# Kernel optimization log

Hardware: AMD Instinct MI355X
Metric: run time of the kernel (lower is better)

Reference implementation:

```python
import jax, jax.numpy as jnp
import numpy as np

B = 4096
L = 15          # self.length
NINP = 256      # emb_size
NHID = 512      # hidden_size
VOCAB = 30005
TOPK = 10
K = 4 * TOPK + 2   # 42 actions
N_SPLIT = 2 * TOPK
N_STEP = 5      # num_edits
PAD = 30003


def _lstm_dir(x, Wih, Whh, b, reverse):
    # x: [T,B,D]; Wih: [4H,D]; Whh: [4H,H]; b: [4H] (b_ih+b_hh). PyTorch gate order i,f,g,o.
    Bsz, H = x.shape[1], Whh.shape[1]
    def step(carry, xt):
        h, c = carry
        z = xt @ Wih.T + h @ Whh.T + b
        i, f, g, o = jnp.split(z, 4, axis=-1)
        c = jax.nn.sigmoid(f) * c + jax.nn.sigmoid(i) * jnp.tanh(g)
        h = jax.nn.sigmoid(o) * jnp.tanh(c)
        return (h, c), h
    h0 = jnp.zeros((Bsz, H), x.dtype)
    _, ys = jax.lax.scan(step, (h0, h0), x, reverse=reverse)
    return ys  # [T,B,H], position-aligned for both directions


def bilstm(x, Wih0, Whh0, b0, Wih1, Whh1, b1):
    # x: [B,T,D] -> [B,T,2H]; 2-layer bidirectional, zero initial state (matches c0/h0 zeros).
    xt = jnp.swapaxes(x, 0, 1)
    for Wih, Whh, b in ((Wih0, Whh0, b0), (Wih1, Whh1, b1)):
        fw = _lstm_dir(xt, Wih[0], Whh[0], b[0], False)
        bw = _lstm_dir(xt, Wih[1], Whh[1], b[1], True)
        xt = jnp.concatenate([fw, bw], axis=-1)
    return jnp.swapaxes(xt, 0, 1)


def policy_step(st_1, length_t, pos, emb0, key_pos, rep_words, valid_id,
                emb_table, enc_table, Wih0, Whh0, b0, Wih1, Whh1, b1,
                del_vec, hold_vec, mlp_W, mlp_b, mlp1_W, mlp1_b):
    Bsz = st_1.shape[0]
    pos_row = jnp.zeros((L,), jnp.float32).at[pos].set(1.0)         # static pos
    pos_tensor = jnp.broadcast_to(pos_row[None, :, None], (Bsz, L, 1))
    embt = emb_table[st_1] * (1.0 - pos_tensor)
    x = jnp.concatenate([embt, emb0, pos_tensor], axis=2)            # [B,L,2*ninp+1]
    out = bilstm(x, Wih0, Whh0, b0, Wih1, Whh1, b1)                  # [B,L,2*nhid]
    pooled = out[:, pos, :]
    representation = jnp.concatenate(
        [pooled, key_pos[:, pos:pos + 1], jnp.broadcast_to(pos_row[None, :], (Bsz, L))], axis=1)
    # external encoder output is detached in the original
    word_emb = jax.lax.stop_gradient(enc_table[rep_words])           # [B,4*topk,ninp]
    emb2 = jnp.concatenate([word_emb,
                            jnp.broadcast_to(del_vec, (Bsz, 1, NINP)),
                            jnp.broadcast_to(hold_vec, (Bsz, 1, NINP))], axis=1)  # [B,K,ninp]
    onehot = jnp.broadcast_to(jnp.eye(K, dtype=jnp.float32)[None], (Bsz, K, K))
    emb2 = jnp.concatenate([emb2, onehot], axis=2)                   # [B,K,ninp+K]
    rep100 = representation @ mlp_W.T + mlp_b                        # [B,100]
    emb100 = emb2 @ mlp1_W.T + mlp1_b                                # [B,K,100]
    score = jnp.einsum('bkd,bd->bk', emb100, rep100)
    policy = jax.nn.softmax(score, axis=1)
    action = jnp.argmax(policy, axis=1, keepdims=True).astype(jnp.int32)  # eval mode
    pi = jnp.take_along_axis(policy, action, axis=1)                 # [B,1]

    rep_b = (action < N_SPLIT).astype(jnp.int32)
    replaceflag = rep_b * valid_id
    ins_b = ((action >= N_SPLIT) & (action < 2 * N_SPLIT)).astype(jnp.int32)
    insertflag = ins_b * valid_id * (length_t + ins_b <= 15).astype(jnp.int32)
    del_b = (action == 2 * N_SPLIT).astype(jnp.int32)
    deleteflag = del_b * valid_id * (length_t - del_b > 2).astype(jnp.int32)
    holdflag = 1 - replaceflag - insertflag - deleteflag

    action_words = jnp.take_along_axis(rep_words, jnp.clip(action, 0, N_SPLIT - 1), axis=1)  # [B,1]
    rep_seq = jnp.concatenate([action_words, st_1[:, pos + 1:]], axis=1)
    ins_seq = jnp.concatenate([action_words, st_1[:, pos:-1]], axis=1)
    padding = jnp.full((Bsz, 1), PAD, dtype=st_1.dtype)
    del_seq = jnp.concatenate([st_1[:, pos + 1:], padding], axis=1)
    hol_seq = st_1[:, pos:]
    new_tail = (rep_seq * replaceflag + ins_seq * insertflag
                + del_seq * deleteflag + hol_seq * holdflag)
    st = st_1.at[:, pos:].set(new_tail)
    length_tt = insertflag + length_t - deleteflag
    return st, pi, action.astype(jnp.float32), length_tt


def setup_inputs() -> dict:
    key = jax.random.key(0)
    ks = jax.random.split(key, 20)
    s = 0.05
    in0 = 2 * NINP + 1
    in1 = 2 * NHID
    inp = {
        'input_ids': jax.random.randint(ks[0], (B, L), 0, 30000, dtype=jnp.int32),
        'key_pos': jax.random.uniform(ks[1], (B, L), dtype=jnp.float32),
        'sequence_length': jax.random.randint(ks[2], (B, 1), 3, 16, dtype=jnp.int32),
        'rep_words_all': jax.random.randint(ks[3], (B, N_STEP, 4 * TOPK), 0, 30000, dtype=jnp.int32),
        'valid_id_all': jax.random.randint(ks[4], (B, N_STEP, 1), 0, 2, dtype=jnp.int32),
        'emb_table': jax.random.normal(ks[5], (VOCAB, NINP), jnp.float32) * s,
        'enc_table': jax.random.normal(ks[6], (VOCAB, NINP), jnp.float32) * s,
        'Wih0': jax.random.normal(ks[7], (2, 4 * NHID, in0), jnp.float32) * s,
        'Whh0': jax.random.normal(ks[8], (2, 4 * NHID, NHID), jnp.float32) * s,
        'b0': jax.random.normal(ks[9], (2, 4 * NHID), jnp.float32) * s,
        'Wih1': jax.random.normal(ks[10], (2, 4 * NHID, in1), jnp.float32) * s,
        'Whh1': jax.random.normal(ks[11], (2, 4 * NHID, NHID), jnp.float32) * s,
        'b1': jax.random.normal(ks[12], (2, 4 * NHID), jnp.float32) * s,
        'del_vec': jax.random.uniform(ks[13], (1, 1, NINP), dtype=jnp.float32),
        'hold_vec': jax.random.uniform(ks[14], (1, 1, NINP), dtype=jnp.float32),
        'mlp_W': jax.random.normal(ks[15], (100, 2 * NHID + 1 + L), jnp.float32) * s,
        'mlp_b': jnp.zeros((100,), jnp.float32),
        'mlp1_W': jax.random.normal(ks[16], (100, NINP + K), jnp.float32) * s,
        'mlp1_b': jnp.zeros((100,), jnp.float32),
    }
    return inp


def reference(input_ids, key_pos, sequence_length, rep_words_all, valid_id_all,
              emb_table, enc_table, Wih0, Whh0, b0, Wih1, Whh1, b1,
              del_vec, hold_vec, mlp_W, mlp_b, mlp1_W, mlp1_b):
    st = input_ids
    emb0 = emb_table[input_ids]            # embedding of s0, computed once
    length_t = sequence_length
    pis, acts = [], []
    for i in range(N_STEP):
        pos = i % (L - 3) + 2              # static per unrolled step
        st, pi, a, length_t = policy_step(
            st, length_t, pos, emb0, key_pos,
            rep_words_all[:, i, :], valid_id_all[:, i, :],
            emb_table, enc_table, Wih0, Whh0, b0, Wih1, Whh1, b1,
            del_vec, hold_vec, mlp_W, mlp_b, mlp1_W, mlp1_b)
        pis.append(pi)
        acts.append(a)
    pis = jnp.concatenate(pis, axis=1)     # [B,N_STEP]
    actions = jnp.concatenate(acts, axis=1)
    return pis, actions, st, length_t
```

## Files before the change

### kernel.cpp

```cpp
#include <hip/hip_runtime.h>

#define B_ 4096
#define L_ 15
#define NSTEP_ 5
#define VOC_ 30005
#define PAD_ 30003

typedef _Float16 f16;
typedef f16  f16x8 __attribute__((ext_vector_type(8)));
typedef float f32x16 __attribute__((ext_vector_type(16)));

__device__ __forceinline__ float sigf(float x){ return 1.0f/(1.0f+expf(-x)); }

#define MFMA_(d,a,b) d = __builtin_amdgcn_mfma_f32_32x32x16_f16(a,b,d,0,0,0)

__device__ __forceinline__ void gll16(const f16* g, f16* l){
  __builtin_amdgcn_global_load_lds(
      (const __attribute__((address_space(1))) void*)g,
      (__attribute__((address_space(3))) void*)l, 16, 0, 0);
}

struct RecParams {
  const f16 *A1h_0,*A1l_0,*A1h_1,*A1l_1;
  const f16 *A2h_0,*A2l_0,*A2h_1,*A2l_1;
  const f16 *Wfh_0,*Wfl_0,*Wfh_1,*Wfl_1;
  const float *bias_0,*bias_1;
  const f16 *embH,*embL,*flagpg;
  const int *st,*ids;
  float *c_0,*c_1,*h2_0,*h2_1;
  f16 *hh_0,*hl_0,*hh_1,*hl_1;
  int lda1, lda2, ldh, ldh2, k1p, k2p, first, gather, t_0, t_1, pos, b0c, act0, act1;
};

__device__ __forceinline__ int swz(int row, int s){
  int u = ((row&7)<<1) | s;
  return ((row>>3)<<8) + ((u ^ (u>>1))<<4);
}

__global__ __launch_bounds__(256,2) void rec_gemm(RecParams p){
  const int bxe = blockIdx.x;
  const int ct4 = bxe & 15;
  const int dir = bxe >> 4;
  if (!(dir ? p.act1 : p.act0)) return;
  const f16* A1h = dir ? p.A1h_1 : p.A1h_0;
  const f16* A1l = dir ? p.A1l_1 : p.A1l_0;
  const f16* A2h = dir ? p.A2h_1 : p.A2h_0;
  const f16* A2l = dir ? p.A2l_1 : p.A2l_0;
  const f16* Wfh = dir ? p.Wfh_1 : p.Wfh_0;
  const f16* Wfl = dir ? p.Wfl_1 : p.Wfl_0;
  const float* bias = dir ? p.bias_1 : p.bias_0;
  float* cbuf = dir ? p.c_1 : p.c_0;
  float* h2   = dir ? p.h2_1 : p.h2_0;
  f16* hhb = dir ? p.hh_1 : p.hh_0;
  f16* hlb = dir ? p.hl_1 : p.hl_0;
  const int tcur = dir ? p.t_1 : p.t_0;

  const int tid  = threadIdx.x;
  const int lane = tid & 63;
  const int w    = tid >> 6;
  const int mbase = blockIdx.y*128;

  __shared__ union {
    float z[128*128];
    f16   stg[3][4][2048];
  } sm;

  f32x16 accM[2][2], accX[2][2];
#pragma unroll
  for (int i=0;i<2;i++)
#pragma unroll
    for (int j=0;j<2;j++)
#pragma unroll
      for (int r=0;r<16;r++){ accM[i][j][r]=0.f; accX[i][j][r]=0.f; }

  const int arow = (w&1)*64 + (lane&31);
  const int fs = lane>>5;
  const int aoff0 = swz(arow,    fs), aoff1 = swz(arow+32, fs);

  const int ct0 = ct4*4 + (w>>1)*2;
  const f16* WfhL = Wfh + (size_t)lane*8;
  const f16* WflL = Wfl + (size_t)lane*8;

  int ug = tid & 15; ug ^= ug>>1; ug ^= ug>>2;
  const int rowS = ((tid>>4)<<3) + (ug>>1);
  const int sS   = ug & 1;
  const int ktot = p.k1p + p.k2p;

  int tokT=0, tokI=0, zflag=0;
  if (p.gather){
    int gb = p.b0c + mbase + rowS;
    tokT = p.st [gb*L_ + tcur];
    tokI = p.ids[gb*L_ + tcur];
    zflag = (tcur == p.pos) ? 1 : 0;
  }
  const f16* zeros = p.flagpg + 8;
  const f16* ones0 = p.flagpg;

  auto stage = [&](int ph, int buf){
    f16* d0 = &sm.stg[buf][0][w<<9];
    f16* d1 = &sm.stg[buf][1][w<<9];
    f16* d2 = &sm.stg[buf][2][w<<9];
    f16* d3 = &sm.stg[buf][3][w<<9];
    if (ph < p.k1p){
      if (p.gather){
        if (ph < 8){
          if (zflag){ gll16(zeros,d0); gll16(zeros,d1); gll16(zeros,d2); gll16(zeros,d3); }
          else {
            size_t base = (size_t)tokT*256 + ph*32 + sS*8;
            gll16(p.embH+base, d0); gll16(p.embL+base, d1);
            gll16(p.embH+base+16, d2); gll16(p.embL+base+16, d3);
          }
        } else if (ph < 16){
          size_t base = (size_t)tokI*256 + (ph-8)*32 + sS*8;
          gll16(p.embH+base, d0); gll16(p.embL+base, d1);
          gll16(p.embH+base+16, d2); gll16(p.embL+base+16, d3);
        } else {
          const f16* s0 = (sS==0 && zflag) ? ones0 : zeros;
          gll16(s0,d0); gll16(zeros,d1); gll16(zeros,d2); gll16(zeros,d3);
        }
      } else {
        long base = (long)(mbase+rowS)*p.lda1 + ph*32 + sS*8;
        gll16(A1h+base, d0); gll16(A1l+base, d1);
        gll16(A1h+base+16, d2); gll16(A1l+base+16, d3);
      }
    } else {
      long base = (long)(mbase+rowS)*p.lda2 + (ph - p.k1p)*32 + sS*8;
      gll16(A2h+base, d0); gll16(A2l+base, d1);
      gll16(A2h+base+16, d2); gll16(A2l+base+16, d3);
    }
  };
  auto loadB = [&](int kt16, f16x8* r){
    size_t base = ((size_t)kt16*64 + ct0)*512;
    r[0] = *(const f16x8*)(WfhL + base);
    r[1] = *(const f16x8*)(WfhL + base + 512);
    r[2] = *(const f16x8*)(WflL + base);
    r[3] = *(const f16x8*)(WflL + base + 512);
  };

  f16x8 rb0[4], rb1[4];
  stage(0,0); stage(1,1);
  loadB(0, rb0);
  asm volatile("s_waitcnt vmcnt(8)" ::: "memory");
  __builtin_amdgcn_s_barrier();
  __builtin_amdgcn_sched_barrier(0);

  int bR = 0;
  for (int ph=0; ph<ktot; ++ph){
    const char* s0h = (const char*)sm.stg[bR][0];
    const char* s0l = (const char*)sm.stg[bR][1];
    const char* s1h = (const char*)sm.stg[bR][2];
    const char* s1l = (const char*)sm.stg[bR][3];
    f16x8 a00h = *(const f16x8*)(s0h + aoff0);
    f16x8 a01h = *(const f16x8*)(s0h + aoff1);
    f16x8 a00l = *(const f16x8*)(s0l + aoff0);
    f16x8 a01l = *(const f16x8*)(s0l + aoff1);
    f16x8 a10h = *(const f16x8*)(s1h + aoff0);
    f16x8 a11h = *(const f16x8*)(s1h + aoff1);
    f16x8 a10l = *(const f16x8*)(s1l + aoff0);
    f16x8 a11l = *(const f16x8*)(s1l + aoff1);
    loadB(2*ph+1, rb1);
    if (ph+2 < ktot) stage(ph+2, (bR+2>=3)?(bR-1):(bR+2));
    __builtin_amdgcn_s_setprio(1);
    MFMA_(accM[0][0], a00h, rb0[0]); MFMA_(accX[0][0], a00h, rb0[2]); MFMA_(accX[0][0], a00l, rb0[0]);
    MFMA_(accM[1][0], a01h, rb0[0]); MFMA_(accX[1][0], a01h, rb0[2]); MFMA_(accX[1][0], a01l, rb0[0]);
    MFMA_(accM[0][1], a00h, rb0[1]); MFMA_(accX[0][1], a00h, rb0[3]); MFMA_(accX[0][1], a00l, rb0[1]);
    MFMA_(accM[1][1], a01h, rb0[1]); MFMA_(accX[1][1], a01h, rb0[3]); MFMA_(accX[1][1], a01l, rb0[1]);
    MFMA_(accM[0][0], a10h, rb1[0]); MFMA_(accX[0][0], a10h, rb1[2]); MFMA_(accX[0][0], a10l, rb1[0]);
    MFMA_(accM[1][0], a11h, rb1[0]); MFMA_(accX[1][0], a11h, rb1[2]); MFMA_(accX[1][0], a11l, rb1[0]);
    MFMA_(accM[0][1], a10h, rb1[1]); MFMA_(accX[0][1], a10h, rb1[3]); MFMA_(accX[0][1], a10l, rb1[1]);
    MFMA_(accM[1][1], a11h, rb1[1]); MFMA_(accX[1][1], a11h, rb1[3]); MFMA_(accX[1][1], a11l, rb1[1]);
    __builtin_amdgcn_s_setprio(0);
    if (ph+1 < ktot) loadB(2*ph+2, rb0);
    asm volatile("s_waitcnt vmcnt(8) lgkmcnt(0)" ::: "memory");
    __builtin_amdgcn_s_barrier();
    __builtin_amdgcn_sched_barrier(0);
    bR = (bR+1==3)?0:(bR+1);
  }

  __syncthreads();

#pragma unroll
  for (int tm=0;tm<2;tm++)
#pragma unroll
   for (int tn=0;tn<2;tn++){
    int lcol = (w>>1)*64 + tn*32 + (lane&31);
    float bv = bias[ct4*128 + lcol];
#pragma unroll
    for (int r=0;r<16;r++){
      int lrow = (w&1)*64 + tm*32 + (r&3) + 8*(r>>2) + 4*(lane>>5);
      sm.z[lrow*128 + lcol] = accM[tm][tn][r] + 0.000244140625f*accX[tm][tn][r] + bv;
    }
   }
  __syncthreads();

  const int nb = ct4*32;
#pragma unroll
  for (int it=0; it<16; ++it){
    int idx = it*256 + tid;
    int nq = idx & 31, row = idx >> 5;
    float4 g4 = *(const float4*)&sm.z[row*128 + nq*4];
    int m = mbase + row, n = nb + nq;
    float cp = p.first ? 0.f : cbuf[(size_t)m*512 + n];
    float cc = sigf(g4.y)*cp + sigf(g4.x)*tanhf(g4.z);
    float hv = sigf(g4.w)*tanhf(cc);
    cbuf[(size_t)m*512 + n] = cc;
    f16 hi = (f16)hv;
    f16 lo = (f16)((hv - (float)hi)*4096.0f);
    hhb[(size_t)m*p.ldh + n] = hi;
    hlb[(size_t)m*p.ldh + n] = lo;
    if (h2) h2[(size_t)m*p.ldh2 + n] = hv;
  }
}

__global__ void prep_w0(const float* Wih, const float* Whh, const float* b0,
                        f16* Wfh, f16* Wfl, float* bp){
  int gid = blockIdx.x*blockDim.x + threadIdx.x;
  const int PER_DIR = 66*64*64*8;
  if (gid >= 2*PER_DIR) return;
  int dir = gid / PER_DIR;
  int rem = gid % PER_DIR;
  int j = rem & 7, lane = (rem>>3)&63, ct = (rem>>9)&63, kt16 = rem>>15;
  int n4g = ct*32 + (lane&31);
  int n = n4g>>2, g = n4g&3;
  int srow = dir*2048 + g*512 + n;
  int k = kt16*16 + ((lane>>5)<<3) + j;
  float v;
  if (k < 513)       v = Wih[(size_t)srow*513 + k];
  else if (k < 544)  v = 0.f;
  else               v = Whh[(size_t)srow*512 + (k-544)];
  f16 hi = (f16)v;
  Wfh[gid] = hi;
  Wfl[gid] = (f16)((v - (float)hi)*4096.0f);
  if (kt16==0 && (lane>>5)==0 && j==0) bp[dir*2048 + n4g] = b0[srow];
}

__global__ void prep_w1(const float* Wih, const float* Whh, const float* b1,
                        f16* Wfh, f16* Wfl, float* bp){
  int gid = blockIdx.x*blockDim.x + threadIdx.x;
  const int PER_DIR = 96*64*64*8;
  if (gid >= 2*PER_DIR) return;
  int dir = gid / PER_DIR;
  int rem = gid % PER_DIR;
  int j = rem & 7, lane = (rem>>3)&63, ct = (rem>>9)&63, kt16 = rem>>15;
  int n4g = ct*32 + (lane&31);
  int n = n4g>>2, g = n4g&3;
  int srow = dir*2048 + g*512 + n;
  int k = kt16*16 + ((lane>>5)<<3) + j;
  float v;
  if (k < 1024) v = Wih[(size_t)srow*1024 + k];
  else          v = Whh[(size_t)srow*512 + (k-1024)];
  f16 hi = (f16)v;
  Wfh[gid] = hi;
  Wfl[gid] = (f16)((v - (float)hi)*4096.0f);
  if (kt16==0 && (lane>>5)==0 && j==0) bp[dir*2048 + n4g] = b1[srow];
}

__global__ void prep_emb(const float* emb, f16* eh, f16* el){
  int gid = blockIdx.x*blockDim.x + threadIdx.x;
  if (gid >= VOC_*256) return;
  float v = emb[gid];
  f16 hi = (f16)v;
  eh[gid] = hi;
  el[gid] = (f16)((v - (float)hi)*4096.0f);
}

__global__ void prep_mlpwt(const float* mW, float* wt){
  int gid = blockIdx.x*blockDim.x + threadIdx.x;
  if (gid >= 100*1040) return;
  int j = gid / 1040, k = gid % 1040;
  wt[k*100 + j] = mW[gid];
}

__global__ __launch_bounds__(128) void prep_encproj(const float* enc, const float* delv,
                        const float* holdv, const float* m1W, const float* m1b, float* ep){
  int r = blockIdx.x;
  __shared__ float row[256];
  const float* src = (r < VOC_) ? enc + (size_t)r*256 : (r == VOC_ ? delv : holdv);
  for (int i=threadIdx.x;i<256;i+=128) row[i]=src[i];
  __syncthreads();
  int j = threadIdx.x;
  if (j < 100){
    double s = (double)m1b[j];
    const float* wr = m1W + (size_t)j*298;
    for (int k=0;k<256;k++) s += (double)wr[k] * (double)row[k];
    ep[(size_t)r*100 + j] = (float)s;
  }
}

__global__ void init_st(const int* ids, const int* seqlen, int* st, int* len, f16* flagpg){
  int gid = blockIdx.x*blockDim.x + threadIdx.x;
  if (gid < B_*L_) st[gid] = ids[gid];
  if (gid < B_)    len[gid] = seqlen[gid];
  if (gid < 16)    flagpg[gid] = (gid==0) ? (f16)1.0f : (f16)0.0f;
}

__global__ void sentinel(float* out, float v){
  int gid = blockIdx.x*blockDim.x + threadIdx.x;
  if (gid < B_*NSTEP_) out[gid] = v;
}

__global__ __launch_bounds__(128) void score_update(
    const float* pooled, const float* keypos, const float* mWt, const float* mb,
    const float* ep, const float* m1W, const int* repw, const int* valid,
    int* st, int* len, float* outPis, float* outActs, int step, int pos, int b0){
  int b = blockIdx.x;
  int bg = b0 + b;
  __shared__ float rep[1040];
  __shared__ float r100[100];
  __shared__ double sc[42];
  int tid = threadIdx.x;
  for (int i=tid;i<1024;i+=128) rep[i] = pooled[(size_t)b*1024+i];
  if (tid < 16){
    if (tid == 0) rep[1024] = keypos[bg*L_+pos];
    else          rep[1024+tid] = ((tid-1)==pos) ? 1.f : 0.f;
  }
  __syncthreads();
  if (tid < 100){
    double s = (double)mb[tid];
    for (int k=0;k<1040;k++) s += (double)mWt[k*100+tid] * (double)rep[k];
    r100[tid] = (float)s;
  }
  __syncthreads();
  if (tid < 42){
    int row = (tid < 40) ? repw[((size_t)bg*NSTEP_+step)*40 + tid] : (VOC_ + (tid-40));
    const float* er = ep + (size_t)row*100;
    double s = 0.0;
    for (int j=0;j<100;j++) s += (double)er[j] * (double)r100[j];
    for (int j=0;j<100;j++) s += (double)m1W[j*298 + 256 + tid] * (double)r100[j];
    sc[tid] = s;
  }
  __syncthreads();
  if (tid == 0){
    double mx = sc[0]; int am = 0;
    for (int k=1;k<42;k++) if (sc[k] > mx){ mx = sc[k]; am = k; }
    double sum = 0.0;
    for (int k=0;k<42;k++) sum += exp(sc[k]-mx);
    float pi = (float)(1.0/sum);
    int vid = valid[bg*NSTEP_+step];
    int ln  = len[bg];
    int repb = (am < 20) ? 1 : 0;
    int insb = (am >= 20 && am < 40) ? 1 : 0;
    int delb = (am == 40) ? 1 : 0;
    int repf = repb*vid;
    int insf = insb*vid*(((ln+insb) <= 15) ? 1 : 0);
    int delf = delb*vid*(((ln-delb) >  2) ? 1 : 0);
    int T = L_ - pos;
    int tail[13];
    for (int j=0;j<T;j++) tail[j] = st[bg*L_+pos+j];
    int aw = repw[((size_t)bg*NSTEP_+step)*40 + (am < 20 ? am : 19)];
    for (int j=0;j<T;j++){
      int rv = (j==0) ? aw : tail[j];
      int iv = (j==0) ? aw : tail[j-1];
      int dv = (j < T-1) ? tail[j+1] : PAD_;
      int hv = tail[j];
      int nv = repf ? rv : (insf ? iv : (delf ? dv : hv));
      st[bg*L_+pos+j] = nv;
    }
    len[bg] = ln + insf - delf;
    outPis[bg*NSTEP_+step]  = pi;
    outActs[bg*NSTEP_+step] = (float)am;
  }
}

__global__ void finalize(const int* st, const int* len, float* out){
  int gid = blockIdx.x*blockDim.x + threadIdx.x;
  if (gid < B_*L_)            out[2*B_*NSTEP_ + gid] = (float)st[gid];
  else if (gid < B_*L_ + B_)  out[2*B_*NSTEP_ + B_*L_ + (gid - B_*L_)] = (float)len[gid - B_*L_];
}

extern "C" void kernel_launch(void* const* d_in, const int* in_sizes, int n_in,
                              void* d_out, int out_size, void* d_ws, size_t ws_size,
                              hipStream_t stream) {
  const int*   ids    = (const int*)  d_in[0];
  const float* keypos = (const float*)d_in[1];
  const int*   seqlen = (const int*)  d_in[2];
  const int*   repw   = (const int*)  d_in[3];
  const int*   valid  = (const int*)  d_in[4];
  const float* emb    = (const float*)d_in[5];
  const float* enc    = (const float*)d_in[6];
  const float* Wih0   = (const float*)d_in[7];
  const float* Whh0   = (const float*)d_in[8];
  const float* b0     = (const float*)d_in[9];
  const float* Wih1   = (const float*)d_in[10];
  const float* Whh1   = (const float*)d_in[11];
  const float* b1     = (const float*)d_in[12];
  const float* delv   = (const float*)d_in[13];
  const float* holdv  = (const float*)d_in[14];
  const float* mW     = (const float*)d_in[15];
  const float* mb     = (const float*)d_in[16];
  const float* m1W    = (const float*)d_in[17];
  const float* m1b    = (const float*)d_in[18];
  float* out = (float*)d_out;

  const size_t W0PD = (size_t)66*64*64*8;
  const size_t W1PD = (size_t)96*64*64*8;

  char* ws = (char*)d_ws;
  size_t off = 0;
  auto allocB = [&](size_t bytes) -> char* {
    char* pp = ws + off; off += (bytes + 255) & ~size_t(255); return pp;
  };
  f16*  Wf0h = (f16*)allocB(2*W0PD*2);
  f16*  Wf0l = (f16*)allocB(2*W0PD*2);
  f16*  Wf1h = (f16*)allocB(2*W1PD*2);
  f16*  Wf1l = (f16*)allocB(2*W1PD*2);
  float* bp0 = (float*)allocB(4096*4);
  float* bp1 = (float*)allocB(4096*4);
  f16*  embH = (f16*)allocB((size_t)VOC_*256*2);
  f16*  embL = (f16*)allocB((size_t)VOC_*256*2);
  float* mWt = (float*)allocB(104000*4);
  float* ep  = (float*)allocB((size_t)30007*100*4);
  int* stbuf  = (int*)allocB(B_*L_*4);
  int* lenbuf = (int*)allocB(B_*4);
  f16* flagpg = (f16*)allocB(256);
  size_t fixedB = off;

  const int cands[6] = {4096, 2048, 1024, 512, 256, 128};
  int Bc = 0;
  for (int ci=0; ci<6; ++ci){
    size_t c = cands[ci];
    size_t chunkB = c*(size_t)(15*1024*2*2 + 4*512*2*2 + 2*512*4 + 2*512*4 + 1024*4) + 8*256;
    if (fixedB + chunkB <= ws_size){ Bc = (int)c; break; }
  }
  if (!Bc){
    float code = 100000.0f + (float)(ws_size >> 20);
    sentinel<<<(B_*NSTEP_+255)/256,256,0,stream>>>(out, code);
    return;
  }
  f16* o0h = (f16*)allocB((size_t)L_*Bc*1024*2);
  f16* o0l = (f16*)allocB((size_t)L_*Bc*1024*2);
  f16* h1h = (f16*)allocB((size_t)4*Bc*512*2);
  f16* h1l = (f16*)allocB((size_t)4*Bc*512*2);
  float* c0 = (float*)allocB((size_t)2*Bc*512*4);
  float* c1 = (float*)allocB((size_t)2*Bc*512*4);
  float* pooled = (float*)allocB((size_t)Bc*1024*4);

  prep_w0<<<(int)((2*W0PD+255)/256),256,0,stream>>>(Wih0, Whh0, b0, Wf0h, Wf0l, bp0);
  prep_w1<<<(int)((2*W1PD+255)/256),256,0,stream>>>(Wih1, Whh1, b1, Wf1h, Wf1l, bp1);
  prep_emb<<<(VOC_*256+255)/256,256,0,stream>>>(emb, embH, embL);
  prep_mlpwt<<<(100*1040+255)/256,256,0,stream>>>(mW, mWt);
  prep_encproj<<<30007,128,0,stream>>>(enc, delv, holdv, m1W, m1b, ep);
  init_st<<<(B_*L_+255)/256,256,0,stream>>>(ids, seqlen, stbuf, lenbuf, flagpg);

  for (int b0c=0; b0c<B_; b0c+=Bc){
    for (int step=0; step<NSTEP_; ++step){
      int pos = step + 2;

      for (int ts=0; ts<L_; ++ts){
        int tf = ts, tb = 14-ts;
        RecParams p{};
        p.gather = 1; p.t_0 = tf; p.t_1 = tb; p.pos = pos; p.b0c = b0c;
        p.embH = embH; p.embL = embL; p.flagpg = flagpg; p.st = stbuf; p.ids = ids;
        p.k1p = 17; p.k2p = ts ? 16 : 0;
        size_t of0 = (size_t)(ts?tf-1:0)*Bc*1024;
        size_t of1 = (size_t)(ts?tb+1:0)*Bc*1024 + (ts?512:0);
        p.A2h_0 = o0h + of0;  p.A2l_0 = o0l + of0;
        p.A2h_1 = o0h + of1;  p.A2l_1 = o0l + of1;
        p.lda2 = 1024;
        p.Wfh_0 = Wf0h;        p.Wfl_0 = Wf0l;
        p.Wfh_1 = Wf0h + W0PD; p.Wfl_1 = Wf0l + W0PD;
        p.bias_0 = bp0; p.bias_1 = bp0 + 2048;
        p.c_0 = c0; p.c_1 = c0 + (size_t)Bc*512;
        p.hh_0 = o0h + (size_t)tf*Bc*1024;       p.hl_0 = o0l + (size_t)tf*Bc*1024;
        p.hh_1 = o0h + (size_t)tb*Bc*1024 + 512; p.hl_1 = o0l + (size_t)tb*Bc*1024 + 512;
        p.ldh = 1024;
        p.h2_0 = nullptr; p.h2_1 = nullptr; p.ldh2 = 1024;
        p.first = (ts==0); p.act0 = 1; p.act1 = 1;
        rec_gemm<<<dim3(32,Bc/128),256,0,stream>>>(p);
      }

      int nL1 = L_ - pos;
      for (int ts=0; ts<nL1; ++ts){
        RecParams p{};
        int tf = ts, tb = 14-ts;
        int parR = (ts-1)&1, parW = ts&1;
        p.gather = 0; p.flagpg = flagpg;
        p.A1h_0 = o0h + (size_t)tf*Bc*1024;  p.A1l_0 = o0l + (size_t)tf*Bc*1024;
        p.A1h_1 = o0h + (size_t)tb*Bc*1024;  p.A1l_1 = o0l + (size_t)tb*Bc*1024;
        p.lda1 = 1024; p.k1p = 32;
        p.k2p  = ts ? 16 : 0;
        size_t r0 = (size_t)(0*2 + (ts?parR:0))*Bc*512;
        size_t r1 = (size_t)(1*2 + (ts?parR:0))*Bc*512;
        p.A2h_0 = h1h + r0; p.A2l_0 = h1l + r0;
        p.A2h_1 = h1h + r1; p.A2l_1 = h1l + r1;
        p.lda2 = 512;
        p.Wfh_0 = Wf1h;        p.Wfl_0 = Wf1l;
        p.Wfh_1 = Wf1h + W1PD; p.Wfl_1 = Wf1l + W1PD;
        p.bias_0 = bp1; p.bias_1 = bp1 + 2048;
        p.c_0 = c1; p.c_1 = c1 + (size_t)Bc*512;
        size_t w0 = (size_t)(0*2 + parW)*Bc*512;
        size_t w1 = (size_t)(1*2 + parW)*Bc*512;
        p.hh_0 = h1h + w0; p.hl_0 = h1l + w0;
        p.hh_1 = h1h + w1; p.hl_1 = h1l + w1;
        p.ldh = 512;
        p.h2_0 = (ts == pos)    ? pooled        : nullptr;
        p.h2_1 = (ts == 14-pos) ? (pooled+512)  : nullptr;
        p.ldh2 = 1024;
        p.first = (ts==0);
        p.act0 = (ts <= pos) ? 1 : 0; p.act1 = 1;
        rec_gemm<<<dim3(32,Bc/128),256,0,stream>>>(p);
      }

      score_update<<<Bc,128,0,stream>>>(pooled, keypos, mWt, mb, ep, m1W, repw, valid,
                                        stbuf, lenbuf, out, out + B_*NSTEP_, step, pos, b0c);
    }
  }
  finalize<<<(B_*L_+B_+255)/256,256,0,stream>>>(stbuf, lenbuf, out);
}
```

Measured before the change: 21.90 ms.

## Restructure rec_gemm staging per-wave and prefetch both B k-slices together

Each wave now stages one of the four hi/lo sub-tiles for all 128 rows (four 16-byte loads per lane over rows), instead of every wave loading all four sub-tiles for a slice of rows. Both k16 B-fragments for a phase are loaded into one 8-register buffer one iteration ahead, replacing the split rb0/rb1 scheme. The MFMA issue order is regrouped to reuse B operands across consecutive instructions, and the 2D grid is flattened to 1D. The intent is better load coalescing and more latency hiding for weight loads, at the cost of more VGPRs and changed wait counts, which could lower occupancy or expose a hazard.

```diff
diff --git a/kernel.cpp b/kernel.cpp
--- a/kernel.cpp
+++ b/kernel.cpp
@@ -38,9 +38,9 @@
 }
 
 __global__ __launch_bounds__(256,2) void rec_gemm(RecParams p){
-  const int bxe = blockIdx.x;
-  const int ct4 = bxe & 15;
-  const int dir = bxe >> 4;
+  const int id  = blockIdx.x;
+  const int ct4 = id & 15;
+  const int dir = (id >> 4) & 1;
   if (!(dir ? p.act1 : p.act0)) return;
   const f16* A1h = dir ? p.A1h_1 : p.A1h_0;
   const f16* A1l = dir ? p.A1l_1 : p.A1l_0;
@@ -58,7 +58,7 @@
   const int tid  = threadIdx.x;
   const int lane = tid & 63;
   const int w    = tid >> 6;
-  const int mbase = blockIdx.y*128;
+  const int mbase = (id >> 5) * 128;
 
   __shared__ union {
     float z[128*128];
@@ -81,75 +81,79 @@
   const f16* WfhL = Wfh + (size_t)lane*8;
   const f16* WflL = Wfl + (size_t)lane*8;
 
-  int ug = tid & 15; ug ^= ug>>1; ug ^= ug>>2;
-  const int rowS = ((tid>>4)<<3) + (ug>>1);
-  const int sS   = ug & 1;
+  const int ksubW = w >> 1;
+  const f16* srcEmb = (w&1) ? p.embL : p.embH;
+  const f16* srcA1  = (w&1) ? A1l : A1h;
+  const f16* srcA2  = (w&1) ? A2l : A2h;
+  int rowQ[4], sQ[4], tokT[4], tokI[4];
+#pragma unroll
+  for (int q=0;q<4;q++){
+    int uu = q*64 + lane;
+    int d = uu & 15; d ^= d>>1; d ^= d>>2;
+    rowQ[q] = ((uu>>4)<<3) + (d>>1);
+    sQ[q]   = d & 1;
+    tokT[q] = 0; tokI[q] = 0;
+  }
+  int zflag = 0;
+  if (p.gather){
+    zflag = (tcur == p.pos) ? 1 : 0;
+#pragma unroll
+    for (int q=0;q<4;q++){
+      int gb = p.b0c + mbase + rowQ[q];
+      tokT[q] = p.st [gb*L_ + tcur];
+      tokI[q] = p.ids[gb*L_ + tcur];
+    }
+  }
+  const f16* ones0 = p.flagpg;
+  const f16* zeros = p.flagpg + 8;
   const int ktot = p.k1p + p.k2p;
 
-  int tokT=0, tokI=0, zflag=0;
-  if (p.gather){
-    int gb = p.b0c + mbase + rowS;
-    tokT = p.st [gb*L_ + tcur];
-    tokI = p.ids[gb*L_ + tcur];
-    zflag = (tcur == p.pos) ? 1 : 0;
-  }
-  const f16* zeros = p.flagpg + 8;
-  const f16* ones0 = p.flagpg;
-
-  auto stage = [&](int ph, int buf){
-    f16* d0 = &sm.stg[buf][0][w<<9];
-    f16* d1 = &sm.stg[buf][1][w<<9];
-    f16* d2 = &sm.stg[buf][2][w<<9];
-    f16* d3 = &sm.stg[buf][3][w<<9];
-    if (ph < p.k1p){
-      if (p.gather){
-        if (ph < 8){
-          if (zflag){ gll16(zeros,d0); gll16(zeros,d1); gll16(zeros,d2); gll16(zeros,d3); }
-          else {
-            size_t base = (size_t)tokT*256 + ph*32 + sS*8;
-            gll16(p.embH+base, d0); gll16(p.embL+base, d1);
-            gll16(p.embH+base+16, d2); gll16(p.embL+base+16, d3);
-          }
-        } else if (ph < 16){
-          size_t base = (size_t)tokI*256 + (ph-8)*32 + sS*8;
-          gll16(p.embH+base, d0); gll16(p.embL+base, d1);
-          gll16(p.embH+base+16, d2); gll16(p.embL+base+16, d3);
+  auto stage = [&](int t, int buf){
+    f16* dst = &sm.stg[buf][w][0];
+#pragma unroll
+    for (int q=0;q<4;q++){
+      int koff = ksubW*16 + sQ[q]*8;
+      const f16* src;
+      if (t < p.k1p){
+        if (p.gather){
+          if (t < 8)       src = zflag ? zeros
+                               : (srcEmb + (size_t)tokT[q]*256 + t*32 + koff);
+          else if (t < 16) src = srcEmb + (size_t)tokI[q]*256 + (t-8)*32 + koff;
+          else             src = (zflag && w==0 && sQ[q]==0) ? ones0 : zeros;
         } else {
-          const f16* s0 = (sS==0 && zflag) ? ones0 : zeros;
-          gll16(s0,d0); gll16(zeros,d1); gll16(zeros,d2); gll16(zeros,d3);
+          src = srcA1 + (size_t)(mbase+rowQ[q])*p.lda1 + t*32 + koff;
         }
       } else {
-        long base = (long)(mbase+rowS)*p.lda1 + ph*32 + sS*8;
-        gll16(A1h+base, d0); gll16(A1l+base, d1);
-        gll16(A1h+base+16, d2); gll16(A1l+base+16, d3);
+        src = srcA2 + (size_t)(mbase+rowQ[q])*p.lda2 + (t - p.k1p)*32 + koff;
       }
-    } else {
-      long base = (long)(mbase+rowS)*p.lda2 + (ph - p.k1p)*32 + sS*8;
-      gll16(A2h+base, d0); gll16(A2l+base, d1);
-      gll16(A2h+base+16, d2); gll16(A2l+base+16, d3);
+      gll16(src, dst + q*512);
     }
   };
-  auto loadB = [&](int kt16, f16x8* r){
-    size_t base = ((size_t)kt16*64 + ct0)*512;
-    r[0] = *(const f16x8*)(WfhL + base);
-    r[1] = *(const f16x8*)(WfhL + base + 512);
-    r[2] = *(const f16x8*)(WflL + base);
-    r[3] = *(const f16x8*)(WflL + base + 512);
+  auto loadB = [&](int t, f16x8* rb){
+    size_t b0 = ((size_t)(2*t+0)*64 + ct0)*512;
+    size_t b1 = ((size_t)(2*t+1)*64 + ct0)*512;
+    rb[0] = *(const f16x8*)(WfhL + b0);
+    rb[1] = *(const f16x8*)(WfhL + b0 + 512);
+    rb[2] = *(const f16x8*)(WflL + b0);
+    rb[3] = *(const f16x8*)(WflL + b0 + 512);
+    rb[4] = *(const f16x8*)(WfhL + b1);
+    rb[5] = *(const f16x8*)(WfhL + b1 + 512);
+    rb[6] = *(const f16x8*)(WflL + b1);
+    rb[7] = *(const f16x8*)(WflL + b1 + 512);
   };
 
-  f16x8 rb0[4], rb1[4];
-  stage(0,0); stage(1,1);
-  loadB(0, rb0);
-  asm volatile("s_waitcnt vmcnt(8)" ::: "memory");
+  f16x8 rb[8];
+  stage(0,0); stage(1,1); loadB(0, rb);
+  asm volatile("s_waitcnt vmcnt(12)" ::: "memory");
   __builtin_amdgcn_s_barrier();
   __builtin_amdgcn_sched_barrier(0);
 
-  int bR = 0;
-  for (int ph=0; ph<ktot; ++ph){
-    const char* s0h = (const char*)sm.stg[bR][0];
-    const char* s0l = (const char*)sm.stg[bR][1];
-    const char* s1h = (const char*)sm.stg[bR][2];
-    const char* s1l = (const char*)sm.stg[bR][3];
+  for (int t=0; t<ktot; ++t){
+    const int cur = t % 3;
+    const char* s0h = (const char*)sm.stg[cur][0];
+    const char* s0l = (const char*)sm.stg[cur][1];
+    const char* s1h = (const char*)sm.stg[cur][2];
+    const char* s1l = (const char*)sm.stg[cur][3];
     f16x8 a00h = *(const f16x8*)(s0h + aoff0);
     f16x8 a01h = *(const f16x8*)(s0h + aoff1);
     f16x8 a00l = *(const f16x8*)(s0l + aoff0);
@@ -158,23 +162,27 @@
     f16x8 a11h = *(const f16x8*)(s1h + aoff1);
     f16x8 a10l = *(const f16x8*)(s1l + aoff0);
     f16x8 a11l = *(const f16x8*)(s1l + aoff1);
-    loadB(2*ph+1, rb1);
-    if (ph+2 < ktot) stage(ph+2, (bR+2>=3)?(bR-1):(bR+2));
+    if (t+2 < ktot) stage(t+2, (t+2)%3);
     __builtin_amdgcn_s_setprio(1);
-    MFMA_(accM[0][0], a00h, rb0[0]); MFMA_(accX[0][0], a00h, rb0[2]); MFMA_(accX[0][0], a00l, rb0[0]);
-    MFMA_(accM[1][0], a01h, rb0[0]); MFMA_(accX[1][0], a01h, rb0[2]); MFMA_(accX[1][0], a01l, rb0[0]);
-    MFMA_(accM[0][1], a00h, rb0[1]); MFMA_(accX[0][1], a00h, rb0[3]); MFMA_(accX[0][1], a00l, rb0[1]);
-    MFMA_(accM[1][1], a01h, rb0[1]); MFMA_(accX[1][1], a01h, rb0[3]); MFMA_(accX[1][1], a01l, rb0[1]);
-    MFMA_(accM[0][0], a10h, rb1[0]); MFMA_(accX[0][0], a10h, rb1[2]); MFMA_(accX[0][0], a10l, rb1[0]);
-    MFMA_(accM[1][0], a11h, rb1[0]); MFMA_(accX[1][0], a11h, rb1[2]); MFMA_(accX[1][0], a11l, rb1[0]);
-    MFMA_(accM[0][1], a10h, rb1[1]); MFMA_(accX[0][1], a10h, rb1[3]); MFMA_(accX[0][1], a10l, rb1[1]);
-    MFMA_(accM[1][1], a11h, rb1[1]); MFMA_(accX[1][1], a11h, rb1[3]); MFMA_(accX[1][1], a11l, rb1[1]);
+    MFMA_(accM[0][0], a00h, rb[0]); MFMA_(accM[1][0], a01h, rb[0]);
+    MFMA_(accM[0][1], a00h, rb[1]); MFMA_(accM[1][1], a01h, rb[1]);
+    MFMA_(accX[0][0], a00h, rb[2]); MFMA_(accX[1][0], a01h, rb[2]);
+    MFMA_(accX[0][1], a00h, rb[3]); MFMA_(accX[1][1], a01h, rb[3]);
+    MFMA_(accX[0][0], a00l, rb[0]); MFMA_(accX[1][0], a01l, rb[0]);
+    MFMA_(accX[0][1], a00l, rb[1]); MFMA_(accX[1][1], a01l, rb[1]);
+    MFMA_(accM[0][0], a10h, rb[4]); MFMA_(accM[1][0], a11h, rb[4]);
+    MFMA_(accM[0][1], a10h, rb[5]); MFMA_(accM[1][1], a11h, rb[5]);
+    MFMA_(accX[0][0], a10h, rb[6]); MFMA_(accX[1][0], a11h, rb[6]);
+    MFMA_(accX[0][1], a10h, rb[7]); MFMA_(accX[1][1], a11h, rb[7]);
+    MFMA_(accX[0][0], a10l, rb[4]); MFMA_(accX[1][0], a11l, rb[4]);
+    MFMA_(accX[0][1], a10l, rb[5]); MFMA_(accX[1][1], a11l, rb[5]);
     __builtin_amdgcn_s_setprio(0);
-    if (ph+1 < ktot) loadB(2*ph+2, rb0);
-    asm volatile("s_waitcnt vmcnt(8) lgkmcnt(0)" ::: "memory");
-    __builtin_amdgcn_s_barrier();
-    __builtin_amdgcn_sched_barrier(0);
-    bR = (bR+1==3)?0:(bR+1);
+    if (t+1 < ktot){
+      loadB(t+1, rb);
+      asm volatile("s_waitcnt vmcnt(8)" ::: "memory");
+      __builtin_amdgcn_s_barrier();
+      __builtin_amdgcn_sched_barrier(0);
+    }
   }
 
   __syncthreads();
@@ -442,6 +450,8 @@
   prep_encproj<<<30007,128,0,stream>>>(enc, delv, holdv, m1W, m1b, ep);
   init_st<<<(B_*L_+255)/256,256,0,stream>>>(ids, seqlen, stbuf, lenbuf, flagpg);
 
+  const int nblk = (Bc/128) * 32;
+
   for (int b0c=0; b0c<B_; b0c+=Bc){
     for (int step=0; step<NSTEP_; ++step){
       int pos = step + 2;
@@ -466,7 +476,7 @@
         p.ldh = 1024;
         p.h2_0 = nullptr; p.h2_1 = nullptr; p.ldh2 = 1024;
         p.first = (ts==0); p.act0 = 1; p.act1 = 1;
-        rec_gemm<<<dim3(32,Bc/128),256,0,stream>>>(p);
+        rec_gemm<<<dim3(nblk),256,0,stream>>>(p);
       }
 
       int nL1 = L_ - pos;
@@ -498,7 +508,7 @@
         p.ldh2 = 1024;
         p.first = (ts==0);
         p.act0 = (ts <= pos) ? 1 : 0; p.act1 = 1;
-        rec_gemm<<<dim3(32,Bc/128),256,0,stream>>>(p);
+        rec_gemm<<<dim3(nblk),256,0,stream>>>(p);
       }
 
       score_update<<<Bc,128,0,stream>>>(pooled, keypos, mWt, mb, ep, m1W, repw, valid,
```

After: 21.37 ms. 2.5% less time.
